# Optimization experiments

Measured on AMD Instinct MI355X. Metric: run time of the kernel, lower is better.

## Reference

```python
import math
import jax, jax.numpy as jnp
import numpy as np

B, S, D, H, P, FF = 64, 100, 768, 8, 8, 3072
HD = D // H
NUM_LAYERS = 4
EPS = 1e-5


def _layernorm(x, g, b):
    m = jnp.mean(x, axis=-1, keepdims=True)
    v = jnp.mean(jnp.square(x - m), axis=-1, keepdims=True)
    return (x - m) * jax.lax.rsqrt(v + EPS) * g + b


def _positional_encoding(seq_len, d_model):
    pos = jnp.arange(seq_len, dtype=jnp.float32)[:, None]
    div = jnp.exp(jnp.arange(0, d_model, 2, dtype=jnp.float32) * (-math.log(10000.0) / d_model))
    pe = jnp.zeros((seq_len, d_model), dtype=jnp.float32)
    pe = pe.at[:, 0::2].set(jnp.sin(pos * div))
    pe = pe.at[:, 1::2].set(jnp.cos(pos * div))
    return pe[None]  # [1, S, D]


def setup_inputs() -> dict:
    key = jax.random.key(0)
    ks = jax.random.split(key, 12)
    s = 0.02
    return {
        "template_seq": jax.random.normal(ks[0], (B, S, D), jnp.float32),
        "param_seq": jax.random.normal(ks[1], (B, S, P, 768), jnp.float32),
        # ParamEncoder (shared across all 4 layers)
        "Wc": jax.random.normal(ks[2], (768, D), jnp.float32) * s,
        "bc": jnp.zeros((D,), jnp.float32),
        "gp": jnp.ones((D,), jnp.float32),
        "bp": jnp.zeros((D,), jnp.float32),
        # FFN (shared)
        "W1": jax.random.normal(ks[3], (D, FF), jnp.float32) * s,
        "b1": jnp.zeros((FF,), jnp.float32),
        "W2": jax.random.normal(ks[4], (FF, D), jnp.float32) * s,
        "b2": jnp.zeros((D,), jnp.float32),
        # LayerNorms (shared)
        "g1": jnp.ones((D,), jnp.float32),
        "bn1": jnp.zeros((D,), jnp.float32),
        "g2": jnp.ones((D,), jnp.float32),
        "bn2": jnp.zeros((D,), jnp.float32),
        # final classifier
        "Wfc": jax.random.normal(ks[5], (D * S, 2), jnp.float32) * s,
        "bfc": jnp.zeros((2,), jnp.float32),
    }


def _layer(src, param_seq, Wc, bc, gp, bp, W1, b1, W2, b2, g1, bn1, g2, bn2):
    inv_sqrt_hd = 1.0 / math.sqrt(HD)
    # ParamEncoder: Linear(768->D) per param vector, mean over params, LayerNorm.
    # Linear is linear => mean-then-project is identical to project-then-mean.
    pooled = jnp.mean(param_seq, axis=2)                  # [B, S, 768]
    param_enc = _layernorm(pooled @ Wc + bc, gp, bp)       # [B, S, D]
    pb = param_enc.reshape(B, S, H, HD).transpose(0, 2, 1, 3)  # [B, H, S, HD]
    param_bias = jnp.einsum('bhqd,bhkd->bhqk', pb, pb) * inv_sqrt_hd
    # attention with q = k = v = src (no projections in the original forward)
    q = src.reshape(B, S, H, HD).transpose(0, 2, 1, 3)     # [B, H, S, HD]
    attn = jnp.einsum('bhqd,bhkd->bhqk', q, q) * inv_sqrt_hd + param_bias
    attn = jax.nn.softmax(attn, axis=-1)
    out = jnp.einsum('bhqk,bhkd->bhqd', attn, q)
    out = out.transpose(0, 2, 1, 3).reshape(B, S, D)
    src = _layernorm(src + out, g1, bn1)
    ffn = jax.nn.gelu(src @ W1 + b1, approximate=False) @ W2 + b2
    return _layernorm(src + ffn, g2, bn2)


def reference(template_seq, param_seq, Wc, bc, gp, bp, W1, b1, W2, b2,
              g1, bn1, g2, bn2, Wfc, bfc):
    x = template_seq + _positional_encoding(S, D)
    for _ in range(NUM_LAYERS):
        x = _layer(x, param_seq, Wc, bc, gp, bp, W1, b1, W2, b2, g1, bn1, g2, bn2)
    return x.reshape(B, S * D) @ Wfc + bfc  # [B, 2]
```

## Files before the change

### kernel.cpp

```cpp
#include <hip/hip_runtime.h>
#include <hip/hip_bf16.h>
#include <math.h>


typedef __attribute__((ext_vector_type(8))) short bf16x8;
typedef __attribute__((ext_vector_type(4))) float f32x4;
typedef __attribute__((ext_vector_type(4))) short short4v;

#define BB 64
#define SS 100
#define DD 768
#define HH 8
#define HD 96
#define FF_ 3072
#define ROWS 6400
#define LN10000 9.210340371976184f

__device__ __forceinline__ void async_copy16(void* lds_dst, const void* gsrc) {
  __builtin_amdgcn_global_load_lds(
      (const __attribute__((address_space(1))) void*)gsrc,
      (__attribute__((address_space(3))) void*)lds_dst, 16, 0, 0);
}

__device__ __forceinline__ float block_sum256(float v, float* sbuf) {
#pragma unroll
  for (int o = 32; o > 0; o >>= 1) v += __shfl_xor(v, o, 64);
  int tid = threadIdx.x;
  __syncthreads();
  if ((tid & 63) == 0) sbuf[tid >> 6] = v;
  __syncthreads();
  return sbuf[0] + sbuf[1] + sbuf[2] + sbuf[3];
}

__device__ __forceinline__ float block_sum192(float v, float* sbuf) {
#pragma unroll
  for (int o = 32; o > 0; o >>= 1) v += __shfl_xor(v, o, 64);
  int tid = threadIdx.x;
  __syncthreads();
  if ((tid & 63) == 0) sbuf[tid >> 6] = v;
  __syncthreads();
  return sbuf[0] + sbuf[1] + sbuf[2];
}

__global__ void convert_transpose(const float* __restrict__ in,
                                  __hip_bfloat16* __restrict__ out,
                                  int K, int N) {
  __shared__ float t[32][33];
  int n0 = blockIdx.x * 32, k0 = blockIdx.y * 32;
  int tid = threadIdx.x;
  int tx = tid & 31, ty = tid >> 5;
#pragma unroll
  for (int j = 0; j < 32; j += 8)
    t[ty + j][tx] = in[(size_t)(k0 + ty + j) * N + n0 + tx];
  __syncthreads();
#pragma unroll
  for (int j = 0; j < 32; j += 8)
    out[(size_t)(n0 + ty + j) * K + k0 + tx] = __float2bfloat16(t[tx][ty + j]);
}

__global__ void pool_mean(const float* __restrict__ ps,
                          __hip_bfloat16* __restrict__ pooled) {
  int idx = blockIdx.x * 256 + threadIdx.x;
  int row = idx / DD, c = idx - row * DD;
  float s = 0.f;
#pragma unroll
  for (int p = 0; p < 8; p++) s += ps[(size_t)(row * 8 + p) * DD + c];
  pooled[idx] = __float2bfloat16(s * 0.125f);
}

__global__ void add_pe(const float* __restrict__ t, float* __restrict__ src) {
  int idx = blockIdx.x * 256 + threadIdx.x;
  int row = idx / DD, c = idx - row * DD;
  int srow = row % SS;
  int c2 = c & ~1;
  float ang = (float)srow * expf((float)c2 * (-LN10000 / (float)DD));
  float pe = (c & 1) ? cosf(ang) : sinf(ang);
  src[idx] = t[idx] + pe;
}

template <bool XB16, bool RESID, bool WB16>
__global__ void ln_row(const float* __restrict__ Xf,
                       const __hip_bfloat16* __restrict__ Xb,
                       const float* __restrict__ R,
                       const float* __restrict__ g, const float* __restrict__ bb,
                       float* __restrict__ of, __hip_bfloat16* __restrict__ ob) {
  int row = blockIdx.x, tid = threadIdx.x;
  size_t base = (size_t)row * DD;
  int c4 = tid * 4;
  float4 v;
  if constexpr (XB16) {
    short4v xv = *(const short4v*)(Xb + base + c4);
    __hip_bfloat16* p = (__hip_bfloat16*)&xv;
    v.x = __bfloat162float(p[0]); v.y = __bfloat162float(p[1]);
    v.z = __bfloat162float(p[2]); v.w = __bfloat162float(p[3]);
  } else {
    v = *(const float4*)(Xf + base + c4);
  }
  if (RESID) {
    float4 rv = *(const float4*)(R + base + c4);
    v.x += rv.x; v.y += rv.y; v.z += rv.z; v.w += rv.w;
  }
  __shared__ float sbuf[3];
  float s = block_sum192(v.x + v.y + v.z + v.w, sbuf);
  float mean = s * (1.0f / DD);
  float dx = v.x - mean, dy = v.y - mean, dz = v.z - mean, dw = v.w - mean;
  float ss = block_sum192(dx * dx + dy * dy + dz * dz + dw * dw, sbuf);
  float rs = rsqrtf(ss * (1.0f / DD) + 1e-5f);
  float4 gv = *(const float4*)(g + c4);
  float4 bv = *(const float4*)(bb + c4);
  float4 y;
  y.x = dx * rs * gv.x + bv.x;
  y.y = dy * rs * gv.y + bv.y;
  y.z = dz * rs * gv.z + bv.z;
  y.w = dw * rs * gv.w + bv.w;
  *(float4*)(of + base + c4) = y;
  if (WB16) {
    __hip_bfloat16 hb[4] = {__float2bfloat16(y.x), __float2bfloat16(y.y),
                            __float2bfloat16(y.z), __float2bfloat16(y.w)};
    *(short4v*)(ob + base + c4) = *(short4v*)hb;
  }
}

__launch_bounds__(256, 2)
__global__ void param_bias_mfma(const float* __restrict__ penc,
                                float* __restrict__ pbias) {
  __shared__ __align__(16) __hip_bfloat16 Qs[128][104];
  const int bh = blockIdx.x;
  const int b = bh >> 3, h = bh & 7;
  const int tid = threadIdx.x;
  const int wave = tid >> 6, lane = tid & 63;
  const int r = lane & 15, quad = lane >> 4;
  const int q8 = quad * 8;
  const int wr = (wave >> 1) * 64, wc = (wave & 1) * 64;
  const float sroot = rsqrtf(9.79795897113f);
  for (int i = tid; i < 128 * HD; i += 256) {
    int s = i / HD, d = i - s * HD;
    float v = (s < SS) ? penc[(size_t)(b * SS + s) * DD + h * HD + d] : 0.f;
    Qs[s][d] = __float2bfloat16(v * sroot);
  }
  __syncthreads();
  f32x4 acc[4][4] = {};
#pragma unroll
  for (int k0 = 0; k0 < HD; k0 += 32) {
    bf16x8 af[4], bfv[4];
#pragma unroll
    for (int mi = 0; mi < 4; mi++)
      af[mi] = *(const bf16x8*)&Qs[wr + mi * 16 + r][k0 + q8];
#pragma unroll
    for (int ni = 0; ni < 4; ni++)
      bfv[ni] = *(const bf16x8*)&Qs[wc + ni * 16 + r][k0 + q8];
#pragma unroll
    for (int mi = 0; mi < 4; mi++)
#pragma unroll
      for (int ni = 0; ni < 4; ni++)
        acc[mi][ni] = __builtin_amdgcn_mfma_f32_16x16x32_bf16(af[mi], bfv[ni],
                                                              acc[mi][ni], 0, 0, 0);
  }
  float* pb = pbias + (size_t)bh * SS * SS;
#pragma unroll
  for (int mi = 0; mi < 4; mi++)
#pragma unroll
    for (int ni = 0; ni < 4; ni++) {
      int col = wc + ni * 16 + r;
      if (col < SS) {
#pragma unroll
        for (int rg = 0; rg < 4; rg++) {
          int row = wr + mi * 16 + quad * 4 + rg;
          if (row < SS) pb[row * SS + col] = acc[mi][ni][rg];
        }
      }
    }
}

__launch_bounds__(256, 2)
__global__ void attn_fused_mfma(const float* __restrict__ src,
                                const float* __restrict__ pbias,
                                __hip_bfloat16* __restrict__ out) {
  __shared__ __align__(16) char umem[128 * 136 * 2];
  __shared__ __align__(16) __hip_bfloat16 Qt[96][136];
  __shared__ float redm[2][128];
  __shared__ float reds[2][128];
  __hip_bfloat16 (*Qs)[104] = (__hip_bfloat16 (*)[104])umem;
  __hip_bfloat16 (*Ps)[136] = (__hip_bfloat16 (*)[136])umem;

  const int bh = blockIdx.x;
  const int b = bh >> 3, h = bh & 7;
  const int tid = threadIdx.x;
  const int wave = tid >> 6, lane = tid & 63;
  const int r = lane & 15, quad = lane >> 4;
  const int q8 = quad * 8;
  const int wr = (wave >> 1) * 64, wc = (wave & 1) * 64;

  const float sroot = rsqrtf(9.79795897113f);
  for (int i = tid; i < SS * HD; i += 256) {
    int s = i / HD, d = i - s * HD;
    float v = src[(size_t)(b * SS + s) * DD + h * HD + d];
    Qs[s][d] = __float2bfloat16(v * sroot);
    Qt[d][s] = __float2bfloat16(v);
  }
  for (int i = tid; i < 28 * HD; i += 256) {
    int s = i / HD, d = i - s * HD;
    Qs[100 + s][d] = __float2bfloat16(0.f);
    Qt[d][100 + s] = __float2bfloat16(0.f);
  }

  const float* pb = pbias + (size_t)bh * SS * SS;
  bool cv[4]; int cols[4];
#pragma unroll
  for (int ni = 0; ni < 4; ni++) { cols[ni] = wc + ni * 16 + r; cv[ni] = cols[ni] < SS; }
  f32x4 acc[4][4];
#pragma unroll
  for (int mi = 0; mi < 4; mi++)
#pragma unroll
    for (int rg = 0; rg < 4; rg++) {
      int row = wr + mi * 16 + quad * 4 + rg;
#pragma unroll
      for (int ni = 0; ni < 4; ni++)
        acc[mi][ni][rg] = (row < SS && cv[ni]) ? pb[row * SS + cols[ni]] : 0.f;
    }
  __syncthreads();

#pragma unroll
  for (int k0 = 0; k0 < HD; k0 += 32) {
    bf16x8 af[4], bfv[4];
#pragma unroll
    for (int mi = 0; mi < 4; mi++)
      af[mi] = *(const bf16x8*)&Qs[wr + mi * 16 + r][k0 + q8];
#pragma unroll
    for (int ni = 0; ni < 4; ni++)
      bfv[ni] = *(const bf16x8*)&Qs[wc + ni * 16 + r][k0 + q8];
#pragma unroll
    for (int mi = 0; mi < 4; mi++)
#pragma unroll
      for (int ni = 0; ni < 4; ni++)
        acc[mi][ni] = __builtin_amdgcn_mfma_f32_16x16x32_bf16(af[mi], bfv[ni],
                                                              acc[mi][ni], 0, 0, 0);
  }

  float mx[4][4];
#pragma unroll
  for (int mi = 0; mi < 4; mi++)
#pragma unroll
    for (int rg = 0; rg < 4; rg++) {
      float m = -1e30f;
#pragma unroll
      for (int ni = 0; ni < 4; ni++)
        if (cv[ni]) m = fmaxf(m, acc[mi][ni][rg]);
#pragma unroll
      for (int o = 1; o < 16; o <<= 1) m = fmaxf(m, __shfl_xor(m, o, 64));
      mx[mi][rg] = m;
    }
  if (r == 0) {
#pragma unroll
    for (int mi = 0; mi < 4; mi++)
#pragma unroll
      for (int rg = 0; rg < 4; rg++)
        redm[wave & 1][wr + mi * 16 + quad * 4 + rg] = mx[mi][rg];
  }
  __syncthreads();

#pragma unroll
  for (int mi = 0; mi < 4; mi++)
#pragma unroll
    for (int rg = 0; rg < 4; rg++) {
      int row = wr + mi * 16 + quad * 4 + rg;
      float rmax = fmaxf(redm[0][row], redm[1][row]);
      float s = 0.f;
#pragma unroll
      for (int ni = 0; ni < 4; ni++) {
        float e = cv[ni] ? __expf(acc[mi][ni][rg] - rmax) : 0.f;
        acc[mi][ni][rg] = e;
        s += e;
      }
#pragma unroll
      for (int o = 1; o < 16; o <<= 1) s += __shfl_xor(s, o, 64);
      if (r == 0) reds[wave & 1][row] = s;
    }
  __syncthreads();

#pragma unroll
  for (int mi = 0; mi < 4; mi++)
#pragma unroll
    for (int rg = 0; rg < 4; rg++) {
      int row = wr + mi * 16 + quad * 4 + rg;
      float inv = 1.0f / (reds[0][row] + reds[1][row]);
#pragma unroll
      for (int ni = 0; ni < 4; ni++)
        Ps[row][cols[ni]] = __float2bfloat16(acc[mi][ni][rg] * inv);
    }
  __syncthreads();

  const int wr2 = (wave >> 1) * 48;
  f32x4 po[3][4] = {};
#pragma unroll
  for (int kk = 0; kk < 128; kk += 32) {
    bf16x8 aq[3], bp[4];
#pragma unroll
    for (int mi = 0; mi < 3; mi++)
      aq[mi] = *(const bf16x8*)&Qt[wr2 + mi * 16 + r][kk + q8];
#pragma unroll
    for (int ni = 0; ni < 4; ni++)
      bp[ni] = *(const bf16x8*)&Ps[wc + ni * 16 + r][kk + q8];
#pragma unroll
    for (int mi = 0; mi < 3; mi++)
#pragma unroll
      for (int ni = 0; ni < 4; ni++)
        po[mi][ni] = __builtin_amdgcn_mfma_f32_16x16x32_bf16(aq[mi], bp[ni],
                                                             po[mi][ni], 0, 0, 0);
  }
#pragma unroll
  for (int mi = 0; mi < 3; mi++)
#pragma unroll
    for (int ni = 0; ni < 4; ni++) {
      int qcol = wc + ni * 16 + r;
      if (qcol < SS) {
        int d0 = wr2 + mi * 16 + quad * 4;
        __hip_bfloat16 hb[4];
#pragma unroll
        for (int rg = 0; rg < 4; rg++) hb[rg] = __float2bfloat16(po[mi][ni][rg]);
        *(short4v*)(out + (size_t)(b * SS + qcol) * DD + h * HD + d0) = *(short4v*)hb;
      }
    }
}

template <int MODE>
__launch_bounds__(256)
__global__ void gemm_bt(const __hip_bfloat16* __restrict__ A,
                        const __hip_bfloat16* __restrict__ Bt,
                        const float* __restrict__ bias,
                        const float* __restrict__ resid,
                        float* __restrict__ outf,
                        __hip_bfloat16* __restrict__ outb,
                        int M, int N, int K) {
  constexpr int BM = 128, BN = 128, BK = 32;
  __shared__ __align__(16) __hip_bfloat16 As[BM * BK];
  __shared__ __align__(16) __hip_bfloat16 Bs[BN * BK];
  const int tid = threadIdx.x;
  const int wave = tid >> 6, lane = tid & 63;
  const int wr = (wave >> 1) * 64, wc = (wave & 1) * 64;
  const int m0 = blockIdx.y * BM, n0 = blockIdx.x * BN;
  const int r = lane & 15, q = lane >> 4;

  f32x4 acc[4][4] = {};

  for (int k0 = 0; k0 < K; k0 += BK) {
#pragma unroll
    for (int j = 0; j < 2; j++) {
      int li = tid + 256 * j;
      int row = li >> 2, cp = li & 3;
      async_copy16(As + li * 8, A + (size_t)(m0 + row) * K + k0 + cp * 8);
      async_copy16(Bs + li * 8, Bt + (size_t)(n0 + row) * K + k0 + cp * 8);
    }
    __syncthreads();
    bf16x8 af[4], bfr[4];
#pragma unroll
    for (int mi = 0; mi < 4; mi++)
      af[mi] = *(const bf16x8*)(As + (wr + mi * 16 + r) * BK + q * 8);
#pragma unroll
    for (int ni = 0; ni < 4; ni++)
      bfr[ni] = *(const bf16x8*)(Bs + (wc + ni * 16 + r) * BK + q * 8);
#pragma unroll
    for (int mi = 0; mi < 4; mi++)
#pragma unroll
      for (int ni = 0; ni < 4; ni++)
        acc[mi][ni] = __builtin_amdgcn_mfma_f32_16x16x32_bf16(af[mi], bfr[ni],
                                                              acc[mi][ni], 0, 0, 0);
    __syncthreads();
  }

#pragma unroll
  for (int mi = 0; mi < 4; mi++) {
#pragma unroll
    for (int ni = 0; ni < 4; ni++) {
      int col = n0 + wc + ni * 16 + r;
      float bv = bias[col];
#pragma unroll
      for (int rg = 0; rg < 4; rg++) {
        int row = m0 + wr + mi * 16 + q * 4 + rg;
        size_t oidx = (size_t)row * N + col;
        float v = acc[mi][ni][rg] + bv;
        if constexpr (MODE == 2) v += resid[oidx];
        if constexpr (MODE == 1) {
          v = 0.5f * v * (1.0f + erff(v * 0.70710678118654752f));
          outb[oidx] = __float2bfloat16(v);
        } else {
          outf[oidx] = v;
        }
      }
    }
  }
}

#define CCHUNK 3072
#define NCHUNK 25
__global__ void classifier_part(const float* __restrict__ x,
                                const float* __restrict__ Wfc,
                                float* __restrict__ part) {
  int chunk = blockIdx.x, b = blockIdx.y, tid = threadIdx.x;
  const float* xb = x + (size_t)b * (SS * DD) + chunk * CCHUNK;
  const float* w = Wfc + 2 * (size_t)chunk * CCHUNK;
  float a0 = 0.f, a1 = 0.f;
  for (int i = tid; i < CCHUNK; i += 256) {
    float xv = xb[i];
    float2 wv = *(const float2*)(w + 2 * i);
    a0 += xv * wv.x;
    a1 += xv * wv.y;
  }
  __shared__ float sbuf[4];
  a0 = block_sum256(a0, sbuf);
  a1 = block_sum256(a1, sbuf);
  if (tid == 0) {
    part[(b * NCHUNK + chunk) * 2] = a0;
    part[(b * NCHUNK + chunk) * 2 + 1] = a1;
  }
}

__global__ void classifier_final(const float* __restrict__ part,
                                 const float* __restrict__ bfc,
                                 float* __restrict__ out) {
  int b = threadIdx.x;
  float a0 = bfc[0], a1 = bfc[1];
#pragma unroll
  for (int c = 0; c < NCHUNK; c++) {
    a0 += part[(b * NCHUNK + c) * 2];
    a1 += part[(b * NCHUNK + c) * 2 + 1];
  }
  out[2 * b] = a0;
  out[2 * b + 1] = a1;
}

extern "C" void kernel_launch(void* const* d_in, const int* in_sizes, int n_in,
                              void* d_out, int out_size, void* d_ws, size_t ws_size,
                              hipStream_t stream) {
  const float* Tmpl = (const float*)d_in[0];
  const float* Pseq = (const float*)d_in[1];
  const float* Wc   = (const float*)d_in[2];
  const float* bc   = (const float*)d_in[3];
  const float* gp   = (const float*)d_in[4];
  const float* bp   = (const float*)d_in[5];
  const float* W1   = (const float*)d_in[6];
  const float* b1   = (const float*)d_in[7];
  const float* W2   = (const float*)d_in[8];
  const float* b2   = (const float*)d_in[9];
  const float* g1   = (const float*)d_in[10];
  const float* bn1  = (const float*)d_in[11];
  const float* g2   = (const float*)d_in[12];
  const float* bn2  = (const float*)d_in[13];
  const float* Wfc  = (const float*)d_in[14];
  const float* bfc  = (const float*)d_in[15];
  float* out = (float*)d_out;
  (void)in_sizes; (void)n_in; (void)out_size; (void)ws_size;

  char* ws = (char*)d_ws;
  size_t off = 0;
  auto alloc = [&](size_t n) { size_t o = off; off += (n + 255) & ~(size_t)255; return o; };

  __hip_bfloat16* Wct = (__hip_bfloat16*)(ws + alloc((size_t)768 * 768 * 2));
  __hip_bfloat16* W1t = (__hip_bfloat16*)(ws + alloc((size_t)768 * 3072 * 2));
  __hip_bfloat16* W2t = (__hip_bfloat16*)(ws + alloc((size_t)3072 * 768 * 2));
  size_t h1_off = alloc((size_t)ROWS * FF_ * 2);
  __hip_bfloat16* h1 = (__hip_bfloat16*)(ws + h1_off);
  float* param_enc = (float*)(ws + h1_off);
  size_t slb_off = alloc((size_t)ROWS * DD * 2);
  __hip_bfloat16* src_ln_bf = (__hip_bfloat16*)(ws + slb_off);
  __hip_bfloat16* pooled = (__hip_bfloat16*)(ws + slb_off);
  size_t ao_off = alloc((size_t)ROWS * DD * 4);
  __hip_bfloat16* attn_out_b = (__hip_bfloat16*)(ws + ao_off);
  float* pe_lin = (float*)(ws + ao_off);
  float* pbias = (float*)(ws + alloc((size_t)512 * SS * SS * 4));
  float* src = (float*)(ws + alloc((size_t)ROWS * DD * 4));
  float* src_ln = (float*)(ws + alloc((size_t)ROWS * DD * 4));
  float* z = (float*)(ws + alloc((size_t)ROWS * DD * 4));
  float* cpart = (float*)(ws + alloc((size_t)BB * NCHUNK * 2 * 4));

  convert_transpose<<<dim3(768 / 32, 768 / 32), 256, 0, stream>>>(Wc, Wct, 768, 768);
  convert_transpose<<<dim3(3072 / 32, 768 / 32), 256, 0, stream>>>(W1, W1t, 768, 3072);
  convert_transpose<<<dim3(768 / 32, 3072 / 32), 256, 0, stream>>>(W2, W2t, 3072, 768);
  pool_mean<<<ROWS * DD / 256, 256, 0, stream>>>(Pseq, pooled);
  gemm_bt<0><<<dim3(DD / 128, ROWS / 128), 256, 0, stream>>>(
      pooled, Wct, bc, nullptr, pe_lin, nullptr, ROWS, DD, 768);
  ln_row<false, false, false><<<ROWS, 192, 0, stream>>>(
      pe_lin, nullptr, nullptr, gp, bp, param_enc, nullptr);
  param_bias_mfma<<<512, 256, 0, stream>>>(param_enc, pbias);
  add_pe<<<ROWS * DD / 256, 256, 0, stream>>>(Tmpl, src);

  for (int l = 0; l < 4; ++l) {
    attn_fused_mfma<<<512, 256, 0, stream>>>(src, pbias, attn_out_b);
    ln_row<true, true, true><<<ROWS, 192, 0, stream>>>(
        nullptr, attn_out_b, src, g1, bn1, src_ln, src_ln_bf);
    gemm_bt<1><<<dim3(FF_ / 128, ROWS / 128), 256, 0, stream>>>(
        src_ln_bf, W1t, b1, nullptr, nullptr, h1, ROWS, FF_, DD);
    gemm_bt<2><<<dim3(DD / 128, ROWS / 128), 256, 0, stream>>>(
        h1, W2t, b2, src_ln, z, nullptr, ROWS, DD, FF_);
    ln_row<false, false, false><<<ROWS, 192, 0, stream>>>(
        z, nullptr, nullptr, g2, bn2, src, nullptr);
  }

  classifier_part<<<dim3(NCHUNK, BB), 256, 0, stream>>>(src, Wfc, cpart);
  classifier_final<<<1, 64, 0, stream>>>(cpart, bfc, out);
}
```

Measured before the change: 1.076 ms.

## Split-K the W2 GEMM, fuse reduction into LayerNorm, use bf16 bias and tanh GELU

The second FFN GEMM (K=3072) is split four ways along K, with the partials written in bf16 and summed by a new kernel that also adds bias and residual and applies LayerNorm. This replaces a 300-block launch with 1200 blocks to fill more CUs and removes the separate residual pass. The attention param-bias is also stored in bf16 to halve its traffic, and the exact erf GELU is replaced by the tanh approximation built on __expf. Rounding partial sums and the bias to bf16 and approximating GELU all add numerical error.

```diff
diff --git a/kernel.cpp b/kernel.cpp
--- a/kernel.cpp
+++ b/kernel.cpp
@@ -14,6 +14,7 @@
 #define HD 96
 #define FF_ 3072
 #define ROWS 6400
+#define KSPLIT 4
 #define LN10000 9.210340371976184f
 
 __device__ __forceinline__ void async_copy16(void* lds_dst, const void* gsrc) {
@@ -121,9 +122,43 @@
   }
 }
 
+__global__ void ln_reduce4(const __hip_bfloat16* __restrict__ part,
+                           const float* __restrict__ R,
+                           const float* __restrict__ bias,
+                           const float* __restrict__ g, const float* __restrict__ bb,
+                           float* __restrict__ of) {
+  int row = blockIdx.x, tid = threadIdx.x;
+  size_t base = (size_t)row * DD;
+  int c4 = tid * 4;
+  float4 v = *(const float4*)(R + base + c4);
+  float4 bi = *(const float4*)(bias + c4);
+  v.x += bi.x; v.y += bi.y; v.z += bi.z; v.w += bi.w;
+#pragma unroll
+  for (int kc = 0; kc < KSPLIT; kc++) {
+    short4v pv = *(const short4v*)(part + (size_t)kc * ROWS * DD + base + c4);
+    __hip_bfloat16* p = (__hip_bfloat16*)&pv;
+    v.x += __bfloat162float(p[0]); v.y += __bfloat162float(p[1]);
+    v.z += __bfloat162float(p[2]); v.w += __bfloat162float(p[3]);
+  }
+  __shared__ float sbuf[3];
+  float s = block_sum192(v.x + v.y + v.z + v.w, sbuf);
+  float mean = s * (1.0f / DD);
+  float dx = v.x - mean, dy = v.y - mean, dz = v.z - mean, dw = v.w - mean;
+  float ss = block_sum192(dx * dx + dy * dy + dz * dz + dw * dw, sbuf);
+  float rs = rsqrtf(ss * (1.0f / DD) + 1e-5f);
+  float4 gv = *(const float4*)(g + c4);
+  float4 bv = *(const float4*)(bb + c4);
+  float4 y;
+  y.x = dx * rs * gv.x + bv.x;
+  y.y = dy * rs * gv.y + bv.y;
+  y.z = dz * rs * gv.z + bv.z;
+  y.w = dw * rs * gv.w + bv.w;
+  *(float4*)(of + base + c4) = y;
+}
+
 __launch_bounds__(256, 2)
 __global__ void param_bias_mfma(const float* __restrict__ penc,
-                                float* __restrict__ pbias) {
+                                __hip_bfloat16* __restrict__ pbias) {
   __shared__ __align__(16) __hip_bfloat16 Qs[128][104];
   const int bh = blockIdx.x;
   const int b = bh >> 3, h = bh & 7;
@@ -156,7 +191,7 @@
         acc[mi][ni] = __builtin_amdgcn_mfma_f32_16x16x32_bf16(af[mi], bfv[ni],
                                                               acc[mi][ni], 0, 0, 0);
   }
-  float* pb = pbias + (size_t)bh * SS * SS;
+  __hip_bfloat16* pb = pbias + (size_t)bh * SS * SS;
 #pragma unroll
   for (int mi = 0; mi < 4; mi++)
 #pragma unroll
@@ -166,7 +201,7 @@
 #pragma unroll
         for (int rg = 0; rg < 4; rg++) {
           int row = wr + mi * 16 + quad * 4 + rg;
-          if (row < SS) pb[row * SS + col] = acc[mi][ni][rg];
+          if (row < SS) pb[row * SS + col] = __float2bfloat16(acc[mi][ni][rg]);
         }
       }
     }
@@ -174,7 +209,7 @@
 
 __launch_bounds__(256, 2)
 __global__ void attn_fused_mfma(const float* __restrict__ src,
-                                const float* __restrict__ pbias,
+                                const __hip_bfloat16* __restrict__ pbias,
                                 __hip_bfloat16* __restrict__ out) {
   __shared__ __align__(16) char umem[128 * 136 * 2];
   __shared__ __align__(16) __hip_bfloat16 Qt[96][136];
@@ -204,7 +239,7 @@
     Qt[d][100 + s] = __float2bfloat16(0.f);
   }
 
-  const float* pb = pbias + (size_t)bh * SS * SS;
+  const __hip_bfloat16* pb = pbias + (size_t)bh * SS * SS;
   bool cv[4]; int cols[4];
 #pragma unroll
   for (int ni = 0; ni < 4; ni++) { cols[ni] = wc + ni * 16 + r; cv[ni] = cols[ni] < SS; }
@@ -216,7 +251,8 @@
       int row = wr + mi * 16 + quad * 4 + rg;
 #pragma unroll
       for (int ni = 0; ni < 4; ni++)
-        acc[mi][ni][rg] = (row < SS && cv[ni]) ? pb[row * SS + cols[ni]] : 0.f;
+        acc[mi][ni][rg] = (row < SS && cv[ni])
+                              ? __bfloat162float(pb[row * SS + cols[ni]]) : 0.f;
     }
   __syncthreads();
 
@@ -328,7 +364,6 @@
 __global__ void gemm_bt(const __hip_bfloat16* __restrict__ A,
                         const __hip_bfloat16* __restrict__ Bt,
                         const float* __restrict__ bias,
-                        const float* __restrict__ resid,
                         float* __restrict__ outf,
                         __hip_bfloat16* __restrict__ outb,
                         int M, int N, int K) {
@@ -379,13 +414,75 @@
         int row = m0 + wr + mi * 16 + q * 4 + rg;
         size_t oidx = (size_t)row * N + col;
         float v = acc[mi][ni][rg] + bv;
-        if constexpr (MODE == 2) v += resid[oidx];
         if constexpr (MODE == 1) {
-          v = 0.5f * v * (1.0f + erff(v * 0.70710678118654752f));
-          outb[oidx] = __float2bfloat16(v);
+          float y = 0.79788456080286536f * (v + 0.044715f * v * v * v);
+          float u = __expf(-2.0f * fabsf(y));
+          float th = (1.0f - u) / (1.0f + u);
+          th = copysignf(th, y);
+          float gv2 = 0.5f * v * (1.0f + th);
+          outb[oidx] = __float2bfloat16(gv2);
         } else {
           outf[oidx] = v;
         }
+      }
+    }
+  }
+}
+
+__launch_bounds__(256)
+__global__ void gemm_bt_split(const __hip_bfloat16* __restrict__ A,
+                              const __hip_bfloat16* __restrict__ Bt,
+                              __hip_bfloat16* __restrict__ part,
+                              int M, int N, int K) {
+  constexpr int BM = 128, BN = 128, BK = 32;
+  const int KC = K / KSPLIT;
+  __shared__ __align__(16) __hip_bfloat16 As[BM * BK];
+  __shared__ __align__(16) __hip_bfloat16 Bs[BN * BK];
+  const int tid = threadIdx.x;
+  const int wave = tid >> 6, lane = tid & 63;
+  const int wr = (wave >> 1) * 64, wc = (wave & 1) * 64;
+  const int m0 = blockIdx.y * BM, n0 = blockIdx.x * BN;
+  const int kc = blockIdx.z;
+  const int kbase = kc * KC;
+  const int r = lane & 15, q = lane >> 4;
+
+  f32x4 acc[4][4] = {};
+
+  for (int k0 = 0; k0 < KC; k0 += BK) {
+#pragma unroll
+    for (int j = 0; j < 2; j++) {
+      int li = tid + 256 * j;
+      int row = li >> 2, cp = li & 3;
+      async_copy16(As + li * 8, A + (size_t)(m0 + row) * K + kbase + k0 + cp * 8);
+      async_copy16(Bs + li * 8, Bt + (size_t)(n0 + row) * K + kbase + k0 + cp * 8);
+    }
+    __syncthreads();
+    bf16x8 af[4], bfr[4];
+#pragma unroll
+    for (int mi = 0; mi < 4; mi++)
+      af[mi] = *(const bf16x8*)(As + (wr + mi * 16 + r) * BK + q * 8);
+#pragma unroll
+    for (int ni = 0; ni < 4; ni++)
+      bfr[ni] = *(const bf16x8*)(Bs + (wc + ni * 16 + r) * BK + q * 8);
+#pragma unroll
+    for (int mi = 0; mi < 4; mi++)
+#pragma unroll
+      for (int ni = 0; ni < 4; ni++)
+        acc[mi][ni] = __builtin_amdgcn_mfma_f32_16x16x32_bf16(af[mi], bfr[ni],
+                                                              acc[mi][ni], 0, 0, 0);
+    __syncthreads();
+  }
+
+  __hip_bfloat16* po = part + (size_t)kc * M * N;
+#pragma unroll
+  for (int mi = 0; mi < 4; mi++) {
+#pragma unroll
+    for (int ni = 0; ni < 4; ni++) {
+      int col = n0 + wc + ni * 16 + r;
+#pragma unroll
+      for (int rg = 0; rg < 4; rg++) {
+        int row = m0 + wr + mi * 16 + q * 4 + rg;
+        po[(size_t)row * N + col] = __float2bfloat16(acc[mi][ni][rg]);
       }
     }
   }
@@ -467,10 +564,10 @@
   size_t ao_off = alloc((size_t)ROWS * DD * 4);
   __hip_bfloat16* attn_out_b = (__hip_bfloat16*)(ws + ao_off);
   float* pe_lin = (float*)(ws + ao_off);
-  float* pbias = (float*)(ws + alloc((size_t)512 * SS * SS * 4));
+  __hip_bfloat16* pbias = (__hip_bfloat16*)(ws + alloc((size_t)512 * SS * SS * 2));
   float* src = (float*)(ws + alloc((size_t)ROWS * DD * 4));
   float* src_ln = (float*)(ws + alloc((size_t)ROWS * DD * 4));
-  float* z = (float*)(ws + alloc((size_t)ROWS * DD * 4));
+  __hip_bfloat16* w2part = (__hip_bfloat16*)(ws + alloc((size_t)KSPLIT * ROWS * DD * 2));
   float* cpart = (float*)(ws + alloc((size_t)BB * NCHUNK * 2 * 4));
 
   convert_transpose<<<dim3(768 / 32, 768 / 32), 256, 0, stream>>>(Wc, Wct, 768, 768);
@@ -478,7 +575,7 @@
   convert_transpose<<<dim3(768 / 32, 3072 / 32), 256, 0, stream>>>(W2, W2t, 3072, 768);
   pool_mean<<<ROWS * DD / 256, 256, 0, stream>>>(Pseq, pooled);
   gemm_bt<0><<<dim3(DD / 128, ROWS / 128), 256, 0, stream>>>(
-      pooled, Wct, bc, nullptr, pe_lin, nullptr, ROWS, DD, 768);
+      pooled, Wct, bc, pe_lin, nullptr, ROWS, DD, 768);
   ln_row<false, false, false><<<ROWS, 192, 0, stream>>>(
       pe_lin, nullptr, nullptr, gp, bp, param_enc, nullptr);
   param_bias_mfma<<<512, 256, 0, stream>>>(param_enc, pbias);
@@ -489,11 +586,10 @@
     ln_row<true, true, true><<<ROWS, 192, 0, stream>>>(
         nullptr, attn_out_b, src, g1, bn1, src_ln, src_ln_bf);
     gemm_bt<1><<<dim3(FF_ / 128, ROWS / 128), 256, 0, stream>>>(
-        src_ln_bf, W1t, b1, nullptr, nullptr, h1, ROWS, FF_, DD);
-    gemm_bt<2><<<dim3(DD / 128, ROWS / 128), 256, 0, stream>>>(
-        h1, W2t, b2, src_ln, z, nullptr, ROWS, DD, FF_);
-    ln_row<false, false, false><<<ROWS, 192, 0, stream>>>(
-        z, nullptr, nullptr, g2, bn2, src, nullptr);
+        src_ln_bf, W1t, b1, nullptr, h1, ROWS, FF_, DD);
+    gemm_bt_split<<<dim3(DD / 128, ROWS / 128, KSPLIT), 256, 0, stream>>>(
+        h1, W2t, w2part, ROWS, DD, FF_);
+    ln_reduce4<<<ROWS, 192, 0, stream>>>(w2part, src_ln, b2, g2, bn2, src);
   }
 
   classifier_part<<<dim3(NCHUNK, BB), 256, 0, stream>>>(src, Wfc, cpart);
```

Measured after the change: 1.078 ms. About the same (+0.2%).

## Store param bias in bf16, swizzle GEMM LDS, double K-step, use tanh GELU

Applied to the files above, without the earlier changes.

Param bias is now stored and read as bf16 instead of fp32, halving that buffer's traffic in the attention kernel across all four layers. The GEMM processes 64 K elements per barrier pair, as two 32-wide halves, and XOR-swizzles the 16-byte LDS chunks to reduce bank conflicts on fragment reads. The exact erf GELU is replaced by the tanh approximation computed with a fast exp. These are independent ideas, and the GELU swap and bf16 bias both introduce numerical deviation from the reference.

```diff
diff --git a/kernel.cpp b/kernel.cpp
--- a/kernel.cpp
+++ b/kernel.cpp
@@ -123,7 +123,7 @@
 
 __launch_bounds__(256, 2)
 __global__ void param_bias_mfma(const float* __restrict__ penc,
-                                float* __restrict__ pbias) {
+                                __hip_bfloat16* __restrict__ pbias) {
   __shared__ __align__(16) __hip_bfloat16 Qs[128][104];
   const int bh = blockIdx.x;
   const int b = bh >> 3, h = bh & 7;
@@ -156,7 +156,7 @@
         acc[mi][ni] = __builtin_amdgcn_mfma_f32_16x16x32_bf16(af[mi], bfv[ni],
                                                               acc[mi][ni], 0, 0, 0);
   }
-  float* pb = pbias + (size_t)bh * SS * SS;
+  __hip_bfloat16* pb = pbias + (size_t)bh * SS * SS;
 #pragma unroll
   for (int mi = 0; mi < 4; mi++)
 #pragma unroll
@@ -166,7 +166,7 @@
 #pragma unroll
         for (int rg = 0; rg < 4; rg++) {
           int row = wr + mi * 16 + quad * 4 + rg;
-          if (row < SS) pb[row * SS + col] = acc[mi][ni][rg];
+          if (row < SS) pb[row * SS + col] = __float2bfloat16(acc[mi][ni][rg]);
         }
       }
     }
@@ -174,7 +174,7 @@
 
 __launch_bounds__(256, 2)
 __global__ void attn_fused_mfma(const float* __restrict__ src,
-                                const float* __restrict__ pbias,
+                                const __hip_bfloat16* __restrict__ pbias,
                                 __hip_bfloat16* __restrict__ out) {
   __shared__ __align__(16) char umem[128 * 136 * 2];
   __shared__ __align__(16) __hip_bfloat16 Qt[96][136];
@@ -204,7 +204,7 @@
     Qt[d][100 + s] = __float2bfloat16(0.f);
   }
 
-  const float* pb = pbias + (size_t)bh * SS * SS;
+  const __hip_bfloat16* pb = pbias + (size_t)bh * SS * SS;
   bool cv[4]; int cols[4];
 #pragma unroll
   for (int ni = 0; ni < 4; ni++) { cols[ni] = wc + ni * 16 + r; cv[ni] = cols[ni] < SS; }
@@ -216,7 +216,8 @@
       int row = wr + mi * 16 + quad * 4 + rg;
 #pragma unroll
       for (int ni = 0; ni < 4; ni++)
-        acc[mi][ni][rg] = (row < SS && cv[ni]) ? pb[row * SS + cols[ni]] : 0.f;
+        acc[mi][ni][rg] = (row < SS && cv[ni])
+                              ? __bfloat162float(pb[row * SS + cols[ni]]) : 0.f;
     }
   __syncthreads();
 
@@ -333,38 +334,48 @@
                         __hip_bfloat16* __restrict__ outb,
                         int M, int N, int K) {
   constexpr int BM = 128, BN = 128, BK = 32;
-  __shared__ __align__(16) __hip_bfloat16 As[BM * BK];
-  __shared__ __align__(16) __hip_bfloat16 Bs[BN * BK];
+  __shared__ __align__(16) __hip_bfloat16 As[2][BM * BK];
+  __shared__ __align__(16) __hip_bfloat16 Bs[2][BN * BK];
   const int tid = threadIdx.x;
   const int wave = tid >> 6, lane = tid & 63;
   const int wr = (wave >> 1) * 64, wc = (wave & 1) * 64;
   const int m0 = blockIdx.y * BM, n0 = blockIdx.x * BN;
   const int r = lane & 15, q = lane >> 4;
+  const int qs = (q ^ (r & 3)) * 8;
 
   f32x4 acc[4][4] = {};
 
-  for (int k0 = 0; k0 < K; k0 += BK) {
-#pragma unroll
-    for (int j = 0; j < 2; j++) {
-      int li = tid + 256 * j;
-      int row = li >> 2, cp = li & 3;
-      async_copy16(As + li * 8, A + (size_t)(m0 + row) * K + k0 + cp * 8);
-      async_copy16(Bs + li * 8, Bt + (size_t)(n0 + row) * K + k0 + cp * 8);
+  for (int k0 = 0; k0 < K; k0 += 64) {
+#pragma unroll
+    for (int h = 0; h < 2; h++) {
+#pragma unroll
+      for (int j = 0; j < 2; j++) {
+        int li = tid + 256 * j;
+        int row = li >> 2, cp = li & 3;
+        int cps = cp ^ (row & 3);
+        async_copy16(&As[h][li * 8],
+                     A + (size_t)(m0 + row) * K + k0 + 32 * h + cps * 8);
+        async_copy16(&Bs[h][li * 8],
+                     Bt + (size_t)(n0 + row) * K + k0 + 32 * h + cps * 8);
+      }
     }
     __syncthreads();
-    bf16x8 af[4], bfr[4];
-#pragma unroll
-    for (int mi = 0; mi < 4; mi++)
-      af[mi] = *(const bf16x8*)(As + (wr + mi * 16 + r) * BK + q * 8);
-#pragma unroll
-    for (int ni = 0; ni < 4; ni++)
-      bfr[ni] = *(const bf16x8*)(Bs + (wc + ni * 16 + r) * BK + q * 8);
-#pragma unroll
-    for (int mi = 0; mi < 4; mi++)
-#pragma unroll
-      for (int ni = 0; ni < 4; ni++)
-        acc[mi][ni] = __builtin_amdgcn_mfma_f32_16x16x32_bf16(af[mi], bfr[ni],
-                                                              acc[mi][ni], 0, 0, 0);
+#pragma unroll
+    for (int h = 0; h < 2; h++) {
+      bf16x8 af[4], bfr[4];
+#pragma unroll
+      for (int mi = 0; mi < 4; mi++)
+        af[mi] = *(const bf16x8*)&As[h][(wr + mi * 16 + r) * BK + qs];
+#pragma unroll
+      for (int ni = 0; ni < 4; ni++)
+        bfr[ni] = *(const bf16x8*)&Bs[h][(wc + ni * 16 + r) * BK + qs];
+#pragma unroll
+      for (int mi = 0; mi < 4; mi++)
+#pragma unroll
+        for (int ni = 0; ni < 4; ni++)
+          acc[mi][ni] = __builtin_amdgcn_mfma_f32_16x16x32_bf16(af[mi], bfr[ni],
+                                                                acc[mi][ni], 0, 0, 0);
+    }
     __syncthreads();
   }
 
@@ -381,8 +392,12 @@
         float v = acc[mi][ni][rg] + bv;
         if constexpr (MODE == 2) v += resid[oidx];
         if constexpr (MODE == 1) {
-          v = 0.5f * v * (1.0f + erff(v * 0.70710678118654752f));
-          outb[oidx] = __float2bfloat16(v);
+          float y = 0.79788456080286536f * (v + 0.044715f * v * v * v);
+          float u = __expf(-2.0f * fabsf(y));
+          float th = (1.0f - u) / (1.0f + u);
+          th = copysignf(th, y);
+          float gv2 = 0.5f * v * (1.0f + th);
+          outb[oidx] = __float2bfloat16(gv2);
         } else {
           outf[oidx] = v;
         }
@@ -467,7 +482,7 @@
   size_t ao_off = alloc((size_t)ROWS * DD * 4);
   __hip_bfloat16* attn_out_b = (__hip_bfloat16*)(ws + ao_off);
   float* pe_lin = (float*)(ws + ao_off);
-  float* pbias = (float*)(ws + alloc((size_t)512 * SS * SS * 4));
+  __hip_bfloat16* pbias = (__hip_bfloat16*)(ws + alloc((size_t)512 * SS * SS * 2));
   float* src = (float*)(ws + alloc((size_t)ROWS * DD * 4));
   float* src_ln = (float*)(ws + alloc((size_t)ROWS * DD * 4));
   float* z = (float*)(ws + alloc((size_t)ROWS * DD * 4));
```

After: 1.077 ms. No clear change (+0.1%).
